# Optimization experiments

Measured on AMD Instinct MI355X. Metric: run time of the kernel, lower is better.

## Reference

```python
import jax, jax.numpy as jnp
import numpy as np

DIM = 1024
HEADS = 16
HEAD_DIM = DIM // HEADS
SCALE = HEAD_DIM ** -0.5


def setup_inputs() -> dict:
    key = jax.random.key(0)
    ks = jax.random.split(key, 5)
    B, N, C = 2, 2048, DIM
    x = jax.random.normal(ks[0], (B, N, C), dtype=jnp.float32)
    x2 = jax.random.normal(ks[1], (B, N, C), dtype=jnp.float32)
    # torch nn.Linear weights: [out_features, in_features], no bias (qkv_bias=False)
    s = (1.0 / C) ** 0.5
    Wq = jax.random.uniform(ks[2], (C, C), jnp.float32, -s, s)
    Wa = jax.random.uniform(ks[3], (C, C), jnp.float32, -s, s)
    Wkv = jax.random.uniform(ks[4], (2 * C, C), jnp.float32, -s, s)
    return {"x": x, "x2": x2, "Wq": Wq, "Wa": Wa, "Wkv": Wkv}


def reference(x, x2, Wq, Wa, Wkv):
    B, N, C = x.shape
    H, D = HEADS, HEAD_DIM

    def heads(t):  # [B,N,C] -> [B,H,N,D]
        return t.reshape(B, N, H, D).transpose(0, 2, 1, 3)

    q = heads(x @ Wq.T)
    A = heads(x2 @ Wa.T)
    kv = (x @ Wkv.T).reshape(B, N, 2, H, D).transpose(2, 0, 3, 1, 4)
    k, v = kv[0], kv[1]

    # cascaded double attention (dropout layers in eval mode = identity)
    ATT_q = jax.nn.softmax(jnp.einsum('bhnd,bhmd->bhnm', q, A) * SCALE, axis=-1)
    ATT_k = jax.nn.softmax(jnp.einsum('bhnd,bhmd->bhnm', A, k) * SCALE, axis=-1)
    out = jnp.einsum('bhnm,bhmd->bhnd', ATT_q,
                     jnp.einsum('bhnm,bhmd->bhnd', ATT_k, v))
    return out.transpose(0, 2, 1, 3).reshape(B, N, C)
```

## Files before the change

### kernel.cpp

```cpp
#include <hip/hip_runtime.h>

#define DIM 1024
#define HEADS 16
#define HDIM 64
#define SEQ 2048
#define SCLOG2 0.18033688011112042f

typedef __attribute__((ext_vector_type(8))) short short8;
typedef __attribute__((ext_vector_type(4))) float f32x4;
typedef __attribute__((ext_vector_type(16))) float f32x16;
typedef __attribute__((ext_vector_type(4))) int i32x4;

static __device__ __forceinline__ unsigned short f2bf(float f){
  union { float f; unsigned int u; } v; v.f = f;
  unsigned int r = v.u + 0x7fffu + ((v.u >> 16) & 1u);
  return (unsigned short)(r >> 16);
}

static __device__ __forceinline__ int cvtpk(float lo, float hi){
  int r;
  asm("v_cvt_pk_bf16_f32 %0, %1, %2" : "=v"(r) : "v"(lo), "v"(hi));
  return r;
}
static __device__ __forceinline__ void swap32(int& a, int& b){
  asm("v_permlane32_swap_b32 %0, %1" : "+v"(a), "+v"(b));
}

__device__ __forceinline__ void gl_lds16(const unsigned short* g, unsigned short* l){
  __builtin_amdgcn_global_load_lds((const __attribute__((address_space(1))) void*)g,
                                   (__attribute__((address_space(3))) void*)l, 16, 0, 0);
}

#define CAST_TOTAL 3145728

__global__ __launch_bounds__(256)
void cast_all(const float* __restrict__ x, const float* __restrict__ x2,
              const float* __restrict__ wq, const float* __restrict__ wa,
              const float* __restrict__ wkv, unsigned short* __restrict__ out)
{
  for (int i = blockIdx.x*256 + threadIdx.x; i < CAST_TOTAL; i += gridDim.x*256){
    const float* src; int off;
    if      (i < 1048576){ src = x;   off = i; }
    else if (i < 2097152){ src = x2;  off = i - 1048576; }
    else if (i < 2359296){ src = wq;  off = i - 2097152; }
    else if (i < 2621440){ src = wa;  off = i - 2359296; }
    else                 { src = wkv; off = i - 2621440; }
    float4 v = ((const float4*)src)[off];
    ushort4 o;
    o.x = f2bf(v.x); o.y = f2bf(v.y); o.z = f2bf(v.z); o.w = f2bf(v.w);
    ((ushort4*)out)[i] = o;
  }
}

#define GK 1024

__global__ __launch_bounds__(256)
void gemm_all(const unsigned short* __restrict__ xb,  const unsigned short* __restrict__ x2b,
              const unsigned short* __restrict__ Wqb, const unsigned short* __restrict__ Wab,
              const unsigned short* __restrict__ Wkvb,
              unsigned short* __restrict__ Qw, unsigned short* __restrict__ Aw,
              unsigned short* __restrict__ Kw, unsigned short* __restrict__ Vwt)
{
  __shared__ unsigned short Ald[128*64];
  __shared__ unsigned short Bld[128*64];
  const int tid  = threadIdx.x;
  const int lane = tid & 63;
  const int wid  = tid >> 6;
  const int l15 = lane & 15, l4 = lane >> 4;
  const int wm = wid >> 1, wn = wid & 1;

  const int bid = blockIdx.x;
  const unsigned short *Abuf, *Bbuf;
  int mbase, nbase, isA;
  if (bid < 768){
    int nb = bid % 24, mb = bid / 24;
    nbase = nb*128; mbase = mb*128; isA = 0;
    Abuf = xb;
    Bbuf = (nbase < 1024) ? (Wqb + (size_t)nbase*GK) : (Wkvb + (size_t)(nbase-1024)*GK);
  } else {
    int b2 = bid - 768;
    int nb = b2 & 7, mb = b2 >> 3;
    nbase = nb*128; mbase = mb*128; isA = 1;
    Abuf = x2b;
    Bbuf = Wab + (size_t)nbase*GK;
  }

  const int srow = wid*32 + (lane >> 3);
  const int scol = (lane & 7)*8;
  const unsigned short* gA = Abuf + (size_t)(mbase + srow)*GK + scol;
  const unsigned short* gB = Bbuf + (size_t)srow*GK + scol;
  unsigned short* lA = Ald + (wid*32)*64;
  unsigned short* lB = Bld + (wid*32)*64;

  f32x4 acc[4][4];
  #pragma unroll
  for (int i=0;i<4;i++)
    #pragma unroll
    for(int j=0;j<4;j++) acc[i][j] = (f32x4){0.f,0.f,0.f,0.f};

  for (int kt = 0; kt < GK; kt += 64){
    __syncthreads();
    #pragma unroll
    for (int i=0;i<4;++i){
      gl_lds16(gA + (size_t)(i*8)*GK + kt, lA + i*8*64);
      gl_lds16(gB + (size_t)(i*8)*GK + kt, lB + i*8*64);
    }
    __syncthreads();
    #pragma unroll
    for (int kc = 0; kc < 2; ++kc){
      short8 af[4], bf[4];
      #pragma unroll
      for (int mt=0; mt<4; ++mt)
        af[mt] = *(const short8*)(Ald + (wm*64 + mt*16 + l15)*64 + kc*32 + l4*8);
      #pragma unroll
      for (int nt=0; nt<4; ++nt)
        bf[nt] = *(const short8*)(Bld + (wn*64 + nt*16 + l15)*64 + kc*32 + l4*8);
      #pragma unroll
      for (int mt=0; mt<4; ++mt)
        #pragma unroll
        for (int nt=0; nt<4; ++nt)
          acc[mt][nt] = __builtin_amdgcn_mfma_f32_16x16x32_bf16(af[mt], bf[nt], acc[mt][nt], 0,0,0);
    }
  }

  const float scale = isA ? SCLOG2 : 1.0f;
  #pragma unroll
  for (int mt=0; mt<4; ++mt){
    int mrow = mbase + wm*64 + mt*16 + l4*4;
    int b = mrow >> 11, nblk = mrow & 2047;
    #pragma unroll
    for (int nt=0; nt<4; ++nt){
      int col = nbase + wn*64 + nt*16 + l15;
      if (isA){
        int h = col >> 6, d = col & 63;
        #pragma unroll
        for (int r=0; r<4; ++r)
          Aw[((size_t)((b*HEADS + h)*SEQ + nblk + r))*HDIM + d] = f2bf(acc[mt][nt][r] * scale);
      } else if (col < 1024){
        int h = col >> 6, d = col & 63;
        #pragma unroll
        for (int r=0; r<4; ++r)
          Qw[((size_t)((b*HEADS + h)*SEQ + nblk + r))*HDIM + d] = f2bf(acc[mt][nt][r]);
      } else if (col < 2048){
        int c2 = col - 1024, h = c2 >> 6, d = c2 & 63;
        #pragma unroll
        for (int r=0; r<4; ++r)
          Kw[((size_t)((b*HEADS + h)*SEQ + nblk + r))*HDIM + d] = f2bf(acc[mt][nt][r]);
      } else {
        int c2 = col - 2048, h = c2 >> 6, d = c2 & 63;
        ushort4 pk;
        pk.x = f2bf(acc[mt][nt][0]);
        pk.y = f2bf(acc[mt][nt][1]);
        pk.z = f2bf(acc[mt][nt][2]);
        pk.w = f2bf(acc[mt][nt][3]);
        *(ushort4*)(Vwt + ((size_t)((b*HEADS + h)*HDIM + d))*SEQ + nblk) = pk;
      }
    }
  }
}

#define KT2 64
#define NTH 16

__global__ __launch_bounds__(512)
void attn_pass(const unsigned short* __restrict__ Qb,
               const unsigned short* __restrict__ Kb,
               const unsigned short* __restrict__ Vtb,
               unsigned short* __restrict__ ytb,
               float* __restrict__ outf,
               int mode)
{
  __shared__ __align__(16) char SHRAW[65536];
  unsigned short* SH = (unsigned short*)SHRAW;
  const int tid = threadIdx.x, lane = tid & 63, wid = tid >> 6;
  const int l31 = lane & 31, l5 = lane >> 5;
  const int qw = wid & 3, kvh = wid >> 2;

  const int bid = blockIdx.x;
  const int cx = bid & 7, j = bid >> 3;
  const int bh = cx*4 + (j >> 4);
  const int qb = j & 15;
  const int q0 = qb*128 + qw*32;
  const size_t base = (size_t)bh * SEQ * HDIM;

  short8 qf[4];
  #pragma unroll
  for (int db=0; db<4; ++db)
    qf[db] = *(const short8*)(Qb + base + (size_t)(q0 + l31)*HDIM + db*16 + l5*8);

  const unsigned short* gsrc[4];
  int ldst[4];
  int sstep;
  const int grpoff = kvh * 16384;
  if (qw < 2){
    #pragma unroll
    for (int f=0; f<4; ++f){
      gsrc[f] = Kb + base + (size_t)(kvh*1024 + qw*32 + l31)*HDIM + f*16 + l5*8;
      ldst[f] = grpoff + (qw*4 + f)*512;
    }
    sstep = KT2*HDIM;
  } else {
    const int db2 = qw - 2;
    #pragma unroll
    for (int f=0; f<4; ++f){
      gsrc[f] = Vtb + base + (size_t)(db2*32 + l31)*SEQ + kvh*1024 + f*16 + l5*8;
      ldst[f] = grpoff + 4096 + (db2*4 + f)*512;
    }
    sstep = KT2;
  }

  f32x16 oo0, oo1, ssum;
  #pragma unroll
  for (int r=0;r<16;++r){ oo0[r]=0.f; oo1[r]=0.f; ssum[r]=0.f; }
  short8 ones;
  #pragma unroll
  for (int jj=0;jj<8;++jj) ones[jj] = (short)0x3F80;

  #pragma unroll
  for (int f=0; f<4; ++f)
    gl_lds16(gsrc[f], SH + ldst[f]);
  asm volatile("s_waitcnt vmcnt(0)" ::: "memory");
  __builtin_amdgcn_s_barrier();
  __builtin_amdgcn_sched_barrier(0);

  for (int t = 0; t < NTH; ++t){
    const int cur = t & 1;
    if (t+1 < NTH){
      const int pbuf = ((t+1) & 1) * 8192;
      #pragma unroll
      for (int f=0; f<4; ++f)
        gl_lds16(gsrc[f] + (size_t)(t+1)*sstep, SH + ldst[f] + pbuf);
    }
    const unsigned short* Kc = SH + grpoff + cur*8192;
    const unsigned short* Vc = Kc + 4096;

    float p[32];
    #pragma unroll
    for (int kb=0; kb<2; ++kb){
      f32x16 sacc;
      #pragma unroll
      for (int r=0;r<16;++r) sacc[r]=0.f;
      __builtin_amdgcn_s_setprio(1);
      #pragma unroll
      for (int db=0; db<4; ++db){
        short8 kfr = *(const short8*)(Kc + (kb*4+db)*512 + lane*8);
        sacc = __builtin_amdgcn_mfma_f32_32x32x16_bf16(kfr, qf[db], sacc, 0,0,0);
      }
      __builtin_amdgcn_s_setprio(0);
      #pragma unroll
      for (int r=0;r<16;++r)
        p[kb*16+r] = __builtin_amdgcn_exp2f(sacc[r]);
    }

    #pragma unroll
    for (int kb2=0; kb2<4; ++kb2){
      const int pb = (kb2>>1)*16 + (kb2&1)*8;
      int a0 = cvtpk(p[pb+0], p[pb+1]);
      int b0 = cvtpk(p[pb+4], p[pb+5]);
      int a1 = cvtpk(p[pb+2], p[pb+3]);
      int b1 = cvtpk(p[pb+6], p[pb+7]);
      swap32(a0, b0);
      swap32(a1, b1);
      i32x4 pav; pav[0]=a0; pav[1]=a1; pav[2]=b0; pav[3]=b1;
      short8 paf = *(short8*)&pav;
      __builtin_amdgcn_s_setprio(1);
      ssum = __builtin_amdgcn_mfma_f32_32x32x16_bf16(ones, paf, ssum, 0,0,0);
      short8 v0 = *(const short8*)(Vc + (0*4+kb2)*512 + lane*8);
      oo0 = __builtin_amdgcn_mfma_f32_32x32x16_bf16(v0, paf, oo0, 0,0,0);
      short8 v1 = *(const short8*)(Vc + (1*4+kb2)*512 + lane*8);
      oo1 = __builtin_amdgcn_mfma_f32_32x32x16_bf16(v1, paf, oo1, 0,0,0);
      __builtin_amdgcn_s_setprio(0);
    }

    asm volatile("s_waitcnt vmcnt(0)" ::: "memory");
    __builtin_amdgcn_s_barrier();
    __builtin_amdgcn_sched_barrier(0);
  }

  float* Of  = (float*)SHRAW;
  float* Os1 = (float*)(SHRAW + 128*68*4);
  const int ql = qw*32 + l31;

  if (kvh == 1){
    #pragma unroll
    for (int g=0; g<4; ++g){
      f32x4 w0, w1;
      #pragma unroll
      for (int r=0;r<4;++r){ w0[r] = oo0[g*4+r]; w1[r] = oo1[g*4+r]; }
      int d0 = 8*g + 4*l5;
      *(f32x4*)(Of + ql*68 + d0)      = w0;
      *(f32x4*)(Of + ql*68 + d0 + 32) = w1;
    }
    Os1[ql] = ssum[0];
  }
  __syncthreads();

  if (kvh == 0){
    const float rinv = 1.0f / (ssum[0] + Os1[ql]);
    if (mode == 0){
      #pragma unroll
      for (int r=0;r<16;++r){
        int d0 = (r&3) + 8*(r>>2) + 4*l5;
        float f0 = (oo0[r] + Of[ql*68 + d0])      * rinv;
        float f1 = (oo1[r] + Of[ql*68 + d0 + 32]) * rinv;
        ytb[base + (size_t)(d0)*SEQ + q0 + l31]    = f2bf(f0);
        ytb[base + (size_t)(d0+32)*SEQ + q0 + l31] = f2bf(f1);
      }
    } else {
      #pragma unroll
      for (int g=0; g<4; ++g){
        int d0 = 8*g + 4*l5;
        f32x4 w0 = *(const f32x4*)(Of + ql*68 + d0);
        f32x4 w1 = *(const f32x4*)(Of + ql*68 + d0 + 32);
        #pragma unroll
        for (int r=0;r<4;++r){ w0[r] = (w0[r]+oo0[g*4+r])*rinv; w1[r] = (w1[r]+oo1[g*4+r])*rinv; }
        *(f32x4*)(Of + ql*68 + d0)      = w0;
        *(f32x4*)(Of + ql*68 + d0 + 32) = w1;
      }
    }
  }

  if (mode == 1){
    __syncthreads();
    const int b = bh >> 4, h = bh & 15;
    const int qr = tid >> 2, dh = (tid & 3)*16;
    const float* src = Of + qr*68 + dh;
    float* drow = outf + ((size_t)(b*SEQ + qb*128 + qr))*DIM + h*HDIM + dh;
    #pragma unroll
    for (int k2=0;k2<4;++k2)
      *(float4*)(drow + k2*4) = *(const float4*)(src + k2*4);
  }
}

extern "C" void kernel_launch(void* const* d_in, const int* in_sizes, int n_in,
                              void* d_out, int out_size, void* d_ws, size_t ws_size,
                              hipStream_t stream) {
  const float* x   = (const float*)d_in[0];
  const float* x2  = (const float*)d_in[1];
  const float* Wq  = (const float*)d_in[2];
  const float* Wa  = (const float*)d_in[3];
  const float* Wkv = (const float*)d_in[4];
  float* out = (float*)d_out;

  unsigned short* ws = (unsigned short*)d_ws;
  unsigned short* xb   = ws;
  unsigned short* x2b  = xb   + 4096*1024;
  unsigned short* Wqb  = x2b  + 4096*1024;
  unsigned short* Wab  = Wqb  + 1024*1024;
  unsigned short* Wkvb = Wab  + 1024*1024;
  unsigned short* Qw   = Wkvb + 2048*1024;
  unsigned short* Aw   = Qw   + 4194304;
  unsigned short* Kw   = Aw   + 4194304;
  unsigned short* Vwt  = Kw   + 4194304;
  unsigned short* Ywt  = xb;

  cast_all<<<dim3(3072), dim3(256), 0, stream>>>(x, x2, Wq, Wa, Wkv, ws);

  gemm_all<<<dim3(1024), dim3(256), 0, stream>>>(xb, x2b, Wqb, Wab, Wkvb, Qw, Aw, Kw, Vwt);

  attn_pass<<<dim3(512), dim3(512), 0, stream>>>(Aw, Kw, Vwt, Ywt, nullptr, 0);

  attn_pass<<<dim3(512), dim3(512), 0, stream>>>(Qw, Aw, Ywt, nullptr, out, 1);
}
```

Measured before the change: 157.6 us.

## Double-buffer projection GEMM LDS, remap blocks per XCD, vectorize Q/K/A stores

The projection GEMM now double-buffers its LDS tiles so the global-to-LDS loads for the next K step run while MFMAs consume the current one, with a single barrier per iteration and raised wave priority around the MFMA block. Block indices are remapped so that blocks landing on the same XCD share M rows, aiming for better L2 reuse. For the Q, K and A outputs the MFMA operands are swapped so each lane holds four consecutive head dims and can write a packed ushort4 instead of four scalar strided stores. This doubles LDS use and may lower occupancy.

```diff
diff --git a/kernel.cpp b/kernel.cpp
--- a/kernel.cpp
+++ b/kernel.cpp
@@ -61,8 +61,8 @@
               unsigned short* __restrict__ Qw, unsigned short* __restrict__ Aw,
               unsigned short* __restrict__ Kw, unsigned short* __restrict__ Vwt)
 {
-  __shared__ unsigned short Ald[128*64];
-  __shared__ unsigned short Bld[128*64];
+  __shared__ unsigned short Ald[2][128*64];
+  __shared__ unsigned short Bld[2][128*64];
   const int tid  = threadIdx.x;
   const int lane = tid & 63;
   const int wid  = tid >> 6;
@@ -73,24 +73,27 @@
   const unsigned short *Abuf, *Bbuf;
   int mbase, nbase, isA;
   if (bid < 768){
-    int nb = bid % 24, mb = bid / 24;
+    int xcd = bid & 7, s = bid >> 3;
+    int mb = xcd*4 + (s & 3);
+    int nb = s >> 2;
     nbase = nb*128; mbase = mb*128; isA = 0;
     Abuf = xb;
     Bbuf = (nbase < 1024) ? (Wqb + (size_t)nbase*GK) : (Wkvb + (size_t)(nbase-1024)*GK);
   } else {
     int b2 = bid - 768;
-    int nb = b2 & 7, mb = b2 >> 3;
+    int xcd = b2 & 7, s = b2 >> 3;
+    int mb = xcd*4 + (s & 3);
+    int nb = s >> 2;
     nbase = nb*128; mbase = mb*128; isA = 1;
     Abuf = x2b;
     Bbuf = Wab + (size_t)nbase*GK;
   }
+  const bool isV = (!isA) && (nbase >= 2048);
 
   const int srow = wid*32 + (lane >> 3);
   const int scol = (lane & 7)*8;
   const unsigned short* gA = Abuf + (size_t)(mbase + srow)*GK + scol;
   const unsigned short* gB = Bbuf + (size_t)srow*GK + scol;
-  unsigned short* lA = Ald + (wid*32)*64;
-  unsigned short* lB = Bld + (wid*32)*64;
 
   f32x4 acc[4][4];
   #pragma unroll
@@ -98,55 +101,84 @@
     #pragma unroll
     for(int j=0;j<4;j++) acc[i][j] = (f32x4){0.f,0.f,0.f,0.f};
 
-  for (int kt = 0; kt < GK; kt += 64){
-    __syncthreads();
-    #pragma unroll
-    for (int i=0;i<4;++i){
-      gl_lds16(gA + (size_t)(i*8)*GK + kt, lA + i*8*64);
-      gl_lds16(gB + (size_t)(i*8)*GK + kt, lB + i*8*64);
-    }
-    __syncthreads();
+  #pragma unroll
+  for (int i=0;i<4;++i){
+    gl_lds16(gA + (size_t)(i*8)*GK, &Ald[0][(wid*32 + i*8)*64]);
+    gl_lds16(gB + (size_t)(i*8)*GK, &Bld[0][(wid*32 + i*8)*64]);
+  }
+  asm volatile("s_waitcnt vmcnt(0)" ::: "memory");
+  __builtin_amdgcn_s_barrier();
+  __builtin_amdgcn_sched_barrier(0);
+
+  for (int t = 0; t < 16; ++t){
+    const int cur = t & 1;
+    if (t+1 < 16){
+      const int nxt = cur ^ 1;
+      const int kt = (t+1)*64;
+      #pragma unroll
+      for (int i=0;i<4;++i){
+        gl_lds16(gA + (size_t)(i*8)*GK + kt, &Ald[nxt][(wid*32 + i*8)*64]);
+        gl_lds16(gB + (size_t)(i*8)*GK + kt, &Bld[nxt][(wid*32 + i*8)*64]);
+      }
+    }
     #pragma unroll
     for (int kc = 0; kc < 2; ++kc){
       short8 af[4], bf[4];
       #pragma unroll
       for (int mt=0; mt<4; ++mt)
-        af[mt] = *(const short8*)(Ald + (wm*64 + mt*16 + l15)*64 + kc*32 + l4*8);
+        af[mt] = *(const short8*)(&Ald[cur][(wm*64 + mt*16 + l15)*64 + kc*32 + l4*8]);
       #pragma unroll
       for (int nt=0; nt<4; ++nt)
-        bf[nt] = *(const short8*)(Bld + (wn*64 + nt*16 + l15)*64 + kc*32 + l4*8);
-      #pragma unroll
-      for (int mt=0; mt<4; ++mt)
+        bf[nt] = *(const short8*)(&Bld[cur][(wn*64 + nt*16 + l15)*64 + kc*32 + l4*8]);
+      __builtin_amdgcn_s_setprio(1);
+      if (isV){
         #pragma unroll
-        for (int nt=0; nt<4; ++nt)
-          acc[mt][nt] = __builtin_amdgcn_mfma_f32_16x16x32_bf16(af[mt], bf[nt], acc[mt][nt], 0,0,0);
-    }
-  }
-
-  const float scale = isA ? SCLOG2 : 1.0f;
-  #pragma unroll
-  for (int mt=0; mt<4; ++mt){
-    int mrow = mbase + wm*64 + mt*16 + l4*4;
-    int b = mrow >> 11, nblk = mrow & 2047;
-    #pragma unroll
-    for (int nt=0; nt<4; ++nt){
-      int col = nbase + wn*64 + nt*16 + l15;
-      if (isA){
-        int h = col >> 6, d = col & 63;
+        for (int mt=0; mt<4; ++mt)
+          #pragma unroll
+          for (int nt=0; nt<4; ++nt)
+            acc[mt][nt] = __builtin_amdgcn_mfma_f32_16x16x32_bf16(af[mt], bf[nt], acc[mt][nt], 0,0,0);
+      } else {
         #pragma unroll
-        for (int r=0; r<4; ++r)
-          Aw[((size_t)((b*HEADS + h)*SEQ + nblk + r))*HDIM + d] = f2bf(acc[mt][nt][r] * scale);
-      } else if (col < 1024){
-        int h = col >> 6, d = col & 63;
-        #pragma unroll
-        for (int r=0; r<4; ++r)
-          Qw[((size_t)((b*HEADS + h)*SEQ + nblk + r))*HDIM + d] = f2bf(acc[mt][nt][r]);
-      } else if (col < 2048){
-        int c2 = col - 1024, h = c2 >> 6, d = c2 & 63;
-        #pragma unroll
-        for (int r=0; r<4; ++r)
-          Kw[((size_t)((b*HEADS + h)*SEQ + nblk + r))*HDIM + d] = f2bf(acc[mt][nt][r]);
-      } else {
+        for (int mt=0; mt<4; ++mt)
+          #pragma unroll
+          for (int nt=0; nt<4; ++nt)
+            acc[mt][nt] = __builtin_amdgcn_mfma_f32_16x16x32_bf16(bf[nt], af[mt], acc[mt][nt], 0,0,0);
+      }
+      __builtin_amdgcn_s_setprio(0);
+    }
+    asm volatile("s_waitcnt vmcnt(0)" ::: "memory");
+    __builtin_amdgcn_s_barrier();
+    __builtin_amdgcn_sched_barrier(0);
+  }
+
+  if (!isV){
+    unsigned short* dst = isA ? Aw : (nbase < 1024 ? Qw : Kw);
+    const int coff = (!isA && nbase >= 1024) ? 1024 : 0;
+    const float scale = isA ? SCLOG2 : 1.0f;
+    #pragma unroll
+    for (int mt=0; mt<4; ++mt){
+      int token = mbase + wm*64 + mt*16 + l15;
+      int b = token >> 11, n = token & 2047;
+      #pragma unroll
+      for (int nt=0; nt<4; ++nt){
+        int colb = nbase - coff + wn*64 + nt*16 + l4*4;
+        int h = colb >> 6, d = colb & 63;
+        ushort4 pk;
+        pk.x = f2bf(acc[mt][nt][0] * scale);
+        pk.y = f2bf(acc[mt][nt][1] * scale);
+        pk.z = f2bf(acc[mt][nt][2] * scale);
+        pk.w = f2bf(acc[mt][nt][3] * scale);
+        *(ushort4*)(dst + ((size_t)((b*HEADS + h)*SEQ + n))*HDIM + d) = pk;
+      }
+    }
+  } else {
+    #pragma unroll
+    for (int mt=0; mt<4; ++mt){
+      int mrow = mbase + wm*64 + mt*16 + l4*4;
+      int b = mrow >> 11, nblk = mrow & 2047;
+      #pragma unroll
+      for (int nt=0; nt<4; ++nt){
+        int col = nbase + wn*64 + nt*16 + l15;
         int c2 = col - 2048, h = c2 >> 6, d = c2 & 63;
         ushort4 pk;
         pk.x = f2bf(acc[mt][nt][0]);
```

Measured after the change: 156.8 us. Within noise of the previous version (-0.5%).
